# Kernel tuning notes

Measured on AMD Instinct MI355X. Metric: run time of the kernel, lower is better.

Reference implementation:

```python
import jax, jax.numpy as jnp
import numpy as np

NUM_HEADS = 16


def setup_inputs() -> dict:
    key = jax.random.key(0)
    ks = jax.random.split(key, 7)
    B, S, H = 2, 2048, 1024
    x = jax.random.normal(ks[0], (B, S, H), dtype=jnp.float32)
    y = jax.random.normal(ks[1], (B, S, H), dtype=jnp.float32)
    bias = jnp.zeros((B, 1, 1, S), dtype=jnp.float32)  # additive attention bias (padding mask)
    w_scale = 0.02
    wq = jax.random.normal(ks[2], (H, H), dtype=jnp.float32) * w_scale
    wk = jax.random.normal(ks[3], (H, H), dtype=jnp.float32) * w_scale
    wv = jax.random.normal(ks[4], (H, H), dtype=jnp.float32) * w_scale
    wo = jax.random.normal(ks[5], (H, H), dtype=jnp.float32) * w_scale
    return {"x": x, "y": y, "bias": bias, "wq": wq, "wk": wk, "wv": wv, "wo": wo}


def reference(x, y, bias, wq, wk, wv, wo):
    B, S, H = x.shape
    nh = NUM_HEADS
    dh = H // nh
    # QKV projections, split heads: [B, S, H] -> [B, nh, S, dh]
    q = jnp.einsum("bsh,hd->bsd", x, wq).reshape(B, S, nh, dh).transpose(0, 2, 1, 3)
    k = jnp.einsum("bsh,hd->bsd", y, wk).reshape(B, S, nh, dh).transpose(0, 2, 1, 3)
    v = jnp.einsum("bsh,hd->bsd", y, wv).reshape(B, S, nh, dh).transpose(0, 2, 1, 3)
    # Scale queries (tensor2tensor convention: q *= size_per_head ** -0.5)
    q = q * (dh ** -0.5)
    logits = jnp.einsum("bhqd,bhkd->bhqk", q, k) + bias  # [B, nh, S, S]
    weights = jax.nn.softmax(logits, axis=-1)
    # (attention_dropout = 0.0 -> identity)
    ctx = jnp.einsum("bhqk,bhkd->bhqd", weights, v)  # [B, nh, S, dh]
    ctx = ctx.transpose(0, 2, 1, 3).reshape(B, S, H)  # combine heads
    return jnp.einsum("bsh,hd->bsd", ctx, wo)
```

## Files before the change

### kernel.cpp

```cpp
#include <hip/hip_runtime.h>

using u16 = unsigned short;
using u32 = unsigned int;

typedef __bf16 bf16x8 __attribute__((ext_vector_type(8)));
typedef __bf16 bf16x4 __attribute__((ext_vector_type(4)));
typedef float f32x4 __attribute__((ext_vector_type(4)));
typedef u16 u16x4 __attribute__((ext_vector_type(4)));

#define GLD_LDS16(gp, lp)                                                                 \
  __builtin_amdgcn_global_load_lds((const __attribute__((address_space(1))) void*)(gp),   \
                                   (__attribute__((address_space(3))) void*)(lp), 16, 0, 0)

__device__ __forceinline__ u16 f2b(float f) {
  union { float f; u32 u; } v; v.f = f;
  return (u16)((v.u + 0x7fffu + ((v.u >> 16) & 1u)) >> 16);
}

__device__ __forceinline__ void pl32swap(u32& a, u32& b) {
  asm("v_permlane32_swap_b32 %0, %1" : "+v"(a), "+v"(b));
}
__device__ __forceinline__ void pl16swap(u32& a, u32& b) {
  asm("v_permlane16_swap_b32 %0, %1" : "+v"(a), "+v"(b));
}
__device__ __forceinline__ u32 cvtpk(float lo, float hi) {
  u32 d; asm("v_cvt_pk_bf16_f32 %0, %1, %2" : "=v"(d) : "v"(lo), "v"(hi));
  return d;
}
#define EXP2(x) __builtin_amdgcn_exp2f(x)

__global__ __launch_bounds__(256) void prep(
    const float* __restrict__ w0, const float* __restrict__ w1,
    const float* __restrict__ w2, const float* __restrict__ w3,
    u16* __restrict__ o0, u16* __restrict__ o1,
    u16* __restrict__ o2, u16* __restrict__ o3,
    const float* __restrict__ x, const float* __restrict__ y,
    u16* __restrict__ xb, u16* __restrict__ yb,
    const float* __restrict__ bias, float* __restrict__ bs) {
  __shared__ float tile[64][65];
  int z = blockIdx.z;
  if (z < 4) {
    const float* src; u16* dst;
    switch (z) {
      case 0: src = w0; dst = o0; break;
      case 1: src = w1; dst = o1; break;
      case 2: src = w2; dst = o2; break;
      default: src = w3; dst = o3; break;
    }
    int bx = blockIdx.x * 64, by = blockIdx.y * 64;
    int tx = threadIdx.x & 63, ty = threadIdx.x >> 6;
    for (int r = ty; r < 64; r += 4)
      tile[r][tx] = src[(size_t)(by + r) * 1024 + bx + tx];
    __syncthreads();
    for (int r = ty; r < 64; r += 4)
      dst[(size_t)(bx + r) * 1024 + by + tx] = f2b(tile[tx][r]);
  } else if (z < 6) {
    const float* src = (z == 4) ? x : y;
    u16* dst = (z == 4) ? xb : yb;
    size_t base = ((size_t)(blockIdx.y * 16 + blockIdx.x) * 256 + threadIdx.x) * 8;
    const size_t step = (size_t)256 * 256 * 8, total = (size_t)4096 * 1024;
    for (size_t i = base; i < total; i += step) {
      float4 f0 = *(const float4*)(src + i);
      float4 f1 = *(const float4*)(src + i + 4);
      bf16x8 v;
      v[0] = (__bf16)f0.x; v[1] = (__bf16)f0.y; v[2] = (__bf16)f0.z; v[3] = (__bf16)f0.w;
      v[4] = (__bf16)f1.x; v[5] = (__bf16)f1.y; v[6] = (__bf16)f1.z; v[7] = (__bf16)f1.w;
      *(bf16x8*)(dst + i) = v;
    }
  } else {
    if (blockIdx.x == 0 && blockIdx.y == 0)
      for (int i = threadIdx.x; i < 4096; i += 256)
        bs[i] = bias[i] * 1.44269504088896f;
  }
}

#define BM 128
#define BN 128
#define BK 64

__global__ __launch_bounds__(256) void gemm_qkv(
    const u16* __restrict__ xb, const u16* __restrict__ yb, const u16* __restrict__ wT,
    u16* __restrict__ Qb, u16* __restrict__ Kb, u16* __restrict__ Vb) {
  __shared__ __align__(16) u16 As[BM * BK];
  __shared__ __align__(16) u16 Bs[BN * BK];
  const int K = 1024;
  int region = blockIdx.y >> 3;
  const u16* A = (region == 0) ? xb : yb;
  const u16* BT = wT + (size_t)region * 1024 * 1024;
  float scale = (region == 0) ? 0.125f * 1.44269504088896f : 1.0f;
  int tid = threadIdx.x;
  int wave = tid >> 6, lane = tid & 63;
  int r = lane & 15, kg = lane >> 4;
  int bm = blockIdx.x * BM, bn = (blockIdx.y & 7) * BN;
  int wr = (wave >> 1) * 64, wc = (wave & 1) * 64;
  f32x4 acc[4][4] = {};

  const u16* Ag = A + (size_t)(bm + wave * 32 + (lane >> 3)) * K + (lane & 7) * 8;
  const u16* Bg = BT + (size_t)(bn + wave * 32 + (lane >> 3)) * K + (lane & 7) * 8;
  u16* Asb = As + wave * 32 * BK;
  u16* Bsb = Bs + wave * 32 * BK;

  for (int k0 = 0; k0 < K; k0 += BK) {
#pragma unroll
    for (int c = 0; c < 4; ++c) {
      GLD_LDS16(Ag + (size_t)c * 8 * K + k0, Asb + c * 8 * BK);
      GLD_LDS16(Bg + (size_t)c * 8 * K + k0, Bsb + c * 8 * BK);
    }
    __syncthreads();
#pragma unroll
    for (int kk = 0; kk < 2; ++kk) {
      bf16x8 af[4], bfv[4];
#pragma unroll
      for (int m = 0; m < 4; ++m)
        af[m] = *(const bf16x8*)&As[(wr + m * 16 + r) * BK + kk * 32 + kg * 8];
#pragma unroll
      for (int n = 0; n < 4; ++n)
        bfv[n] = *(const bf16x8*)&Bs[(wc + n * 16 + r) * BK + kk * 32 + kg * 8];
#pragma unroll
      for (int m = 0; m < 4; ++m)
#pragma unroll
        for (int n = 0; n < 4; ++n)
          acc[m][n] = __builtin_amdgcn_mfma_f32_16x16x32_bf16(af[m], bfv[n], acc[m][n], 0, 0, 0);
    }
    __syncthreads();
  }

  if (region == 2) {
#pragma unroll
    for (int m = 0; m < 4; ++m)
#pragma unroll
      for (int n = 0; n < 4; ++n) {
        int row0 = bm + wr + m * 16 + kg * 4;
        int col = bn + wc + n * 16 + r;
        int bb = row0 >> 11, s = row0 & 2047;
        int hh = col >> 6, dd = col & 63;
        u16x4 pk;
#pragma unroll
        for (int i = 0; i < 4; ++i) pk[i] = f2b(acc[m][n][i]);
        *(u16x4*)&Vb[((size_t)(bb * 16 + hh) * 64 + dd) * 2048 + s] = pk;
      }
  } else {
    u16* dst = (region == 0) ? Qb : Kb;
#pragma unroll
    for (int m = 0; m < 4; ++m)
#pragma unroll
      for (int n = 0; n < 4; ++n)
#pragma unroll
        for (int i = 0; i < 4; ++i) {
          int row = bm + wr + m * 16 + kg * 4 + i;
          int col = bn + wc + n * 16 + r;
          dst[(size_t)row * 1024 + col] = f2b(acc[m][n][i] * scale);
        }
  }
}

__global__ __launch_bounds__(256) void gemm_wo(
    const u16* __restrict__ A, const u16* __restrict__ BT, float* __restrict__ Cp,
    float scale) {
  __shared__ __align__(16) u16 As[BM * BK];
  __shared__ __align__(16) u16 Bs[64 * BK];
  const int K = 1024, N = 1024;
  int tid = threadIdx.x;
  int wave = tid >> 6, lane = tid & 63;
  int r = lane & 15, kg = lane >> 4;
  int lhi = lane >> 3, llo = lane & 7;
  int bm = blockIdx.x * BM, bn = blockIdx.y * 64;
  int wr = (wave >> 1) * 64, wc = (wave & 1) * 32;
  f32x4 acc[4][2] = {};

  const u16* Ag = A + (size_t)(bm + wave * 32 + lhi) * K + llo * 8;
  const u16* Bg = BT + (size_t)(bn + wave * 16 + lhi) * K + llo * 8;
  u16* Asb = As + wave * 32 * BK;
  u16* Bsb = Bs + wave * 16 * BK;

  for (int k0 = 0; k0 < K; k0 += BK) {
#pragma unroll
    for (int c = 0; c < 4; ++c)
      GLD_LDS16(Ag + (size_t)c * 8 * K + k0, Asb + c * 8 * BK);
#pragma unroll
    for (int c = 0; c < 2; ++c)
      GLD_LDS16(Bg + (size_t)c * 8 * K + k0, Bsb + c * 8 * BK);
    __syncthreads();
#pragma unroll
    for (int kk = 0; kk < 2; ++kk) {
      bf16x8 af[4], bfv[2];
#pragma unroll
      for (int m = 0; m < 4; ++m)
        af[m] = *(const bf16x8*)&As[(wr + m * 16 + r) * BK + kk * 32 + kg * 8];
#pragma unroll
      for (int n = 0; n < 2; ++n)
        bfv[n] = *(const bf16x8*)&Bs[(wc + n * 16 + r) * BK + kk * 32 + kg * 8];
#pragma unroll
      for (int m = 0; m < 4; ++m)
#pragma unroll
        for (int n = 0; n < 2; ++n)
          acc[m][n] = __builtin_amdgcn_mfma_f32_16x16x32_bf16(af[m], bfv[n], acc[m][n], 0, 0, 0);
    }
    __syncthreads();
  }

#pragma unroll
  for (int m = 0; m < 4; ++m)
#pragma unroll
    for (int n = 0; n < 2; ++n)
#pragma unroll
      for (int i = 0; i < 4; ++i) {
        int row = bm + wr + m * 16 + kg * 4 + i;
        int col = bn + wc + n * 16 + r;
        Cp[(size_t)row * N + col] = acc[m][n][i] * scale;
      }
}

__global__ __launch_bounds__(512) void flash_attn(
    const u16* __restrict__ Q, const u16* __restrict__ Km, const u16* __restrict__ VtG,
    const float* __restrict__ biasS, u16* __restrict__ ctx) {
  const int S = 2048, H = 1024;
  __shared__ __align__(16) u16 Ks[2][64 * 64];
  __shared__ __align__(16) u16 Vs[2][64 * 64];
  int tid = threadIdx.x;
  int wave = tid >> 6, lane = tid & 63;
  int r = lane & 15, kg = lane >> 4;
  int h = blockIdx.x, b = blockIdx.y, qt = blockIdx.z;

  const u16* Qb = Q + (size_t)(b * S + qt * 128 + wave * 16 + r) * H + h * 64 + kg * 8;
  bf16x8 qa[2];
  qa[0] = *(const bf16x8*)(Qb);
  qa[1] = *(const bf16x8*)(Qb + 32);

  int lhi = lane >> 3, llo = lane & 7;
  int ksch = llo ^ lhi;
  const u16* KgB = Km + (size_t)b * S * H + h * 64;
  const u16* VgB = VtG + ((size_t)(b * 16 + h) * 64) * 2048;
  const float* biasB = biasS + (size_t)b * S;

  float m_i = -1e30f, l_i = 0.f;
  f32x4 acc[4] = {};

  auto issueKV = [&](int kv0, int bi) {
    GLD_LDS16(KgB + (size_t)(kv0 + wave * 8 + lhi) * H + ksch * 8,
              &Ks[bi][wave * 8 * 64]);
    GLD_LDS16(VgB + (size_t)(wave * 8 + lhi) * 2048 + kv0 + ksch * 8,
              &Vs[bi][wave * 8 * 64]);
  };
  auto issueB = [&](int kv0, f32x4* bv) {
#pragma unroll
    for (int n = 0; n < 4; ++n)
      bv[n] = *(const f32x4*)(biasB + kv0 + n * 16 + (kg << 2));
  };

  auto compute = [&](const u16* KsB, const u16* VsB, const f32x4* bv) {
    f32x4 sv[4] = {};
    __builtin_amdgcn_s_setprio(1);
#pragma unroll
    for (int kk = 0; kk < 2; ++kk)
#pragma unroll
      for (int n = 0; n < 4; ++n) {
        bf16x8 kb = *(const bf16x8*)&KsB[(n * 16 + r) * 64 +
                                         ((((kk << 2) + kg) ^ (r & 7)) << 3)];
        sv[n] = __builtin_amdgcn_mfma_f32_16x16x32_bf16(kb, qa[kk], sv[n], 0, 0, 0);
      }
    __builtin_amdgcn_s_setprio(0);

    f32x4 s4[4];
#pragma unroll
    for (int n = 0; n < 4; ++n) s4[n] = sv[n] + bv[n];
    float m0 = fmaxf(fmaxf(s4[0][0], s4[0][1]), fmaxf(s4[0][2], s4[0][3]));
    float m1 = fmaxf(fmaxf(s4[1][0], s4[1][1]), fmaxf(s4[1][2], s4[1][3]));
    float m2 = fmaxf(fmaxf(s4[2][0], s4[2][1]), fmaxf(s4[2][2], s4[2][3]));
    float m3 = fmaxf(fmaxf(s4[3][0], s4[3][1]), fmaxf(s4[3][2], s4[3][3]));
    float mx = fmaxf(fmaxf(m0, m1), fmaxf(m2, m3));
    mx = fmaxf(mx, __shfl_xor(mx, 16));
    mx = fmaxf(mx, __shfl_xor(mx, 32));
    float sc = 1.f;
    if (mx > m_i + 8.f) { sc = EXP2(m_i - mx); l_i *= sc; m_i = mx; }
    if (__any(sc != 1.f)) {
#pragma unroll
      for (int i = 0; i < 4; ++i) {
        float sci = __shfl(sc, (lane & 48) | ((kg << 2) + i));
#pragma unroll
        for (int n = 0; n < 4; ++n) acc[n][i] *= sci;
      }
    }
    float rs = 0.f;
    float e[4][4];
#pragma unroll
    for (int n = 0; n < 4; ++n)
#pragma unroll
      for (int i = 0; i < 4; ++i) {
        e[n][i] = EXP2(s4[n][i] - m_i);
        rs += e[n][i];
      }
    rs += __shfl_xor(rs, 16);
    rs += __shfl_xor(rs, 32);
    l_i += rs;

    u32 w[4][2];
#pragma unroll
    for (int n = 0; n < 4; ++n) {
      w[n][0] = cvtpk(e[n][0], e[n][1]);
      w[n][1] = cvtpk(e[n][2], e[n][3]);
    }

    __builtin_amdgcn_s_setprio(1);
#pragma unroll
    for (int kk = 0; kk < 2; ++kk) {
      u32 a0 = w[2 * kk][0], a1 = w[2 * kk][1];
      u32 b0 = w[2 * kk + 1][0], b1 = w[2 * kk + 1][1];
      pl32swap(a0, b0); pl32swap(a1, b1);
      pl16swap(a0, b0); pl16swap(a1, b1);
      union { u32 u[4]; bf16x8 v; } pa;
      pa.u[0] = a0; pa.u[1] = a1; pa.u[2] = b0; pa.u[3] = b1;
#pragma unroll
      for (int n = 0; n < 4; ++n) {
        bf16x8 vb = *(const bf16x8*)&VsB[(n * 16 + r) * 64 +
                                         ((((kk << 2) + kg) ^ (r & 7)) << 3)];
        acc[n] = __builtin_amdgcn_mfma_f32_16x16x32_bf16(pa.v, vb, acc[n], 0, 0, 0);
      }
    }
    __builtin_amdgcn_s_setprio(0);
  };

  f32x4 bp[4], bn2[4];

  issueKV(0, 0); issueB(0, bp);
  __syncthreads();

  for (int t2 = 0; t2 < 16; ++t2) {
    int kv1 = (t2 * 2 + 1) * 64;
    int kv2 = ((t2 * 2 + 2) & 31) * 64;
    issueKV(kv1, 1); issueB(kv1, bn2);
    compute(Ks[0], Vs[0], bp);
    __syncthreads();
    issueKV(kv2, 0); issueB(kv2, bp);
    compute(Ks[1], Vs[1], bn2);
    __syncthreads();
  }

#pragma unroll
  for (int i = 0; i < 4; ++i) {
    float li = __shfl(l_i, (lane & 48) | ((kg << 2) + i));
    float inv = 1.0f / li;
    size_t row = (size_t)(b * S + qt * 128 + wave * 16 + (kg << 2) + i);
#pragma unroll
    for (int n = 0; n < 4; ++n)
      ctx[row * H + h * 64 + n * 16 + r] = f2b(acc[n][i] * inv);
  }
}

extern "C" void kernel_launch(void* const* d_in, const int* in_sizes, int n_in,
                              void* d_out, int out_size, void* d_ws, size_t ws_size,
                              hipStream_t stream) {
  const float* x    = (const float*)d_in[0];
  const float* y    = (const float*)d_in[1];
  const float* bias = (const float*)d_in[2];
  const float* wq   = (const float*)d_in[3];
  const float* wk   = (const float*)d_in[4];
  const float* wv   = (const float*)d_in[5];
  const float* wo   = (const float*)d_in[6];
  float* out = (float*)d_out;

  u16* ws = (u16*)d_ws;
  const size_t WELEM = 1024 * 1024;
  const size_t MELEM = (size_t)4096 * 1024;
  u16* wqT = ws;
  u16* wkT = wqT + WELEM;
  u16* wvT = wkT + WELEM;
  u16* woT = wvT + WELEM;
  u16* Qb  = woT + WELEM;
  u16* Kb  = Qb + MELEM;
  u16* Vb  = Kb + MELEM;
  u16* xb  = Vb + MELEM;
  u16* yb  = xb + MELEM;
  float* bs = (float*)(yb + MELEM);
  u16* Cb  = Qb;

  dim3 blk(256);
  prep<<<dim3(16, 16, 7), blk, 0, stream>>>(wq, wk, wv, wo, wqT, wkT, wvT, woT,
                                            x, y, xb, yb, bias, bs);
  gemm_qkv<<<dim3(32, 24), blk, 0, stream>>>(xb, yb, wqT, Qb, Kb, Vb);
  flash_attn<<<dim3(16, 2, 16), dim3(512), 0, stream>>>(Qb, Kb, Vb, bs, Cb);
  gemm_wo<<<dim3(32, 16), blk, 0, stream>>>(Cb, woT, out, 1.0f);
}
```

Measured before the change: 140.7 us.

## Compute softmax row sums via MFMA with ones and double KV tile per barrier

Replaces the per-tile row-sum reduction (adds plus cross-lane shuffles) with an extra MFMA that multiplies the probability tile by a ones vector and accumulates into a separate accumulator. The KV pipeline now stages 128 keys per buffer (two 64-key sub-tiles), which halves the number of barriers and loop iterations. LDS use doubles to 64 KB per block, which may lower occupancy, and the row sum is now taken from bf16-rounded probabilities rather than the fp32 values.

```diff
diff --git a/kernel.cpp b/kernel.cpp
--- a/kernel.cpp
+++ b/kernel.cpp
@@ -215,8 +215,8 @@
     const u16* __restrict__ Q, const u16* __restrict__ Km, const u16* __restrict__ VtG,
     const float* __restrict__ biasS, u16* __restrict__ ctx) {
   const int S = 2048, H = 1024;
-  __shared__ __align__(16) u16 Ks[2][64 * 64];
-  __shared__ __align__(16) u16 Vs[2][64 * 64];
+  __shared__ __align__(16) u16 Ks[2][2][64 * 64];
+  __shared__ __align__(16) u16 Vs[2][2][64 * 64];
   int tid = threadIdx.x;
   int wave = tid >> 6, lane = tid & 63;
   int r = lane & 15, kg = lane >> 4;
@@ -226,6 +226,10 @@
   bf16x8 qa[2];
   qa[0] = *(const bf16x8*)(Qb);
   qa[1] = *(const bf16x8*)(Qb + 32);
+
+  bf16x8 onesv;
+#pragma unroll
+  for (int j = 0; j < 8; ++j) onesv[j] = (__bf16)1.0f;
 
   int lhi = lane >> 3, llo = lane & 7;
   int ksch = llo ^ lhi;
@@ -233,22 +237,28 @@
   const u16* VgB = VtG + ((size_t)(b * 16 + h) * 64) * 2048;
   const float* biasB = biasS + (size_t)b * S;
 
-  float m_i = -1e30f, l_i = 0.f;
+  float m_i = -1e30f;
   f32x4 acc[4] = {};
+  f32x4 acc_l = {};
 
   auto issueKV = [&](int kv0, int bi) {
-    GLD_LDS16(KgB + (size_t)(kv0 + wave * 8 + lhi) * H + ksch * 8,
-              &Ks[bi][wave * 8 * 64]);
-    GLD_LDS16(VgB + (size_t)(wave * 8 + lhi) * 2048 + kv0 + ksch * 8,
-              &Vs[bi][wave * 8 * 64]);
+#pragma unroll
+    for (int sub = 0; sub < 2; ++sub) {
+      GLD_LDS16(KgB + (size_t)(kv0 + sub * 64 + wave * 8 + lhi) * H + ksch * 8,
+                &Ks[bi][sub][wave * 8 * 64]);
+      GLD_LDS16(VgB + (size_t)(wave * 8 + lhi) * 2048 + kv0 + sub * 64 + ksch * 8,
+                &Vs[bi][sub][wave * 8 * 64]);
+    }
   };
-  auto issueB = [&](int kv0, f32x4* bv) {
-#pragma unroll
-    for (int n = 0; n < 4; ++n)
-      bv[n] = *(const f32x4*)(biasB + kv0 + n * 16 + (kg << 2));
+  auto issueB = [&](int kv0, f32x4 (*bv)[4]) {
+#pragma unroll
+    for (int sub = 0; sub < 2; ++sub)
+#pragma unroll
+      for (int n = 0; n < 4; ++n)
+        bv[sub][n] = *(const f32x4*)(biasB + kv0 + sub * 64 + n * 16 + (kg << 2));
   };
 
-  auto compute = [&](const u16* KsB, const u16* VsB, const f32x4* bv) {
+  auto computeSub = [&](const u16* KsB, const u16* VsB, const f32x4* bv) {
     f32x4 sv[4] = {};
     __builtin_amdgcn_s_setprio(1);
 #pragma unroll
@@ -272,27 +282,22 @@
     mx = fmaxf(mx, __shfl_xor(mx, 16));
     mx = fmaxf(mx, __shfl_xor(mx, 32));
     float sc = 1.f;
-    if (mx > m_i + 8.f) { sc = EXP2(m_i - mx); l_i *= sc; m_i = mx; }
+    if (mx > m_i + 8.f) { sc = EXP2(m_i - mx); m_i = mx; }
     if (__any(sc != 1.f)) {
 #pragma unroll
       for (int i = 0; i < 4; ++i) {
         float sci = __shfl(sc, (lane & 48) | ((kg << 2) + i));
 #pragma unroll
         for (int n = 0; n < 4; ++n) acc[n][i] *= sci;
-      }
-    }
-    float rs = 0.f;
+        acc_l[i] *= sci;
+      }
+    }
     float e[4][4];
 #pragma unroll
     for (int n = 0; n < 4; ++n)
 #pragma unroll
-      for (int i = 0; i < 4; ++i) {
+      for (int i = 0; i < 4; ++i)
         e[n][i] = EXP2(s4[n][i] - m_i);
-        rs += e[n][i];
-      }
-    rs += __shfl_xor(rs, 16);
-    rs += __shfl_xor(rs, 32);
-    l_i += rs;
 
     u32 w[4][2];
 #pragma unroll
@@ -316,30 +321,32 @@
                                          ((((kk << 2) + kg) ^ (r & 7)) << 3)];
         acc[n] = __builtin_amdgcn_mfma_f32_16x16x32_bf16(pa.v, vb, acc[n], 0, 0, 0);
       }
+      acc_l = __builtin_amdgcn_mfma_f32_16x16x32_bf16(pa.v, onesv, acc_l, 0, 0, 0);
     }
     __builtin_amdgcn_s_setprio(0);
   };
 
-  f32x4 bp[4], bn2[4];
+  f32x4 bp[2][4], bn2[2][4];
 
   issueKV(0, 0); issueB(0, bp);
   __syncthreads();
 
-  for (int t2 = 0; t2 < 16; ++t2) {
-    int kv1 = (t2 * 2 + 1) * 64;
-    int kv2 = ((t2 * 2 + 2) & 31) * 64;
-    issueKV(kv1, 1); issueB(kv1, bn2);
-    compute(Ks[0], Vs[0], bp);
-    __syncthreads();
-    issueKV(kv2, 0); issueB(kv2, bp);
-    compute(Ks[1], Vs[1], bn2);
-    __syncthreads();
+  for (int t = 0; t < 16; ++t) {
+    int bi = t & 1;
+    int kvn = ((t + 1) & 15) * 128;
+    issueKV(kvn, bi ^ 1); issueB(kvn, bn2);
+    computeSub(Ks[bi][0], Vs[bi][0], bp[0]);
+    computeSub(Ks[bi][1], Vs[bi][1], bp[1]);
+    __syncthreads();
+#pragma unroll
+    for (int sub = 0; sub < 2; ++sub)
+#pragma unroll
+      for (int n = 0; n < 4; ++n) bp[sub][n] = bn2[sub][n];
   }
 
 #pragma unroll
   for (int i = 0; i < 4; ++i) {
-    float li = __shfl(l_i, (lane & 48) | ((kg << 2) + i));
-    float inv = 1.0f / li;
+    float inv = 1.0f / acc_l[i];
     size_t row = (size_t)(b * S + qt * 128 + wave * 16 + (kg << 2) + i);
 #pragma unroll
     for (int n = 0; n < 4; ++n)
```

After: 152.2 us. 1.08x slower.
